# Performance work log

Hardware: AMD Instinct MI355X
Metric: run time of the kernel (lower is better)

## Reference

```python
import jax, jax.numpy as jnp
import numpy as np

N = 100000
E = 1600000
D_IN = 256
HID = 128
EPS = 1e-5


def setup_inputs() -> dict:
    key = jax.random.key(0)
    ks = jax.random.split(key, 8)
    x = jax.random.normal(ks[0], (N, D_IN), dtype=jnp.float32)
    edge_index = jax.random.randint(ks[1], (2, E), 0, N, dtype=jnp.int64)
    edge_weight = jax.random.uniform(ks[2], (E,), dtype=jnp.float32)
    # GCNConv lin weights (glorot-ish scale) + bias
    W1 = jax.random.normal(ks[3], (D_IN, HID), dtype=jnp.float32) / np.sqrt(D_IN)
    b1 = jnp.zeros((HID,), dtype=jnp.float32)
    W2 = jax.random.normal(ks[4], (HID, HID), dtype=jnp.float32) / np.sqrt(HID)
    b2 = jnp.zeros((HID,), dtype=jnp.float32)
    # BatchNorm affine params
    g1 = jnp.ones((HID,), dtype=jnp.float32)
    be1 = jnp.zeros((HID,), dtype=jnp.float32)
    g2 = jnp.ones((HID,), dtype=jnp.float32)
    be2 = jnp.zeros((HID,), dtype=jnp.float32)
    return {"x": x, "edge_index": edge_index, "edge_weight": edge_weight,
            "W1": W1, "b1": b1, "g1": g1, "be1": be1,
            "W2": W2, "b2": b2, "g2": g2, "be2": be2}


def _gcn_layer(h, src, dst, w, W, b):
    # GCNConv(add_self_loops=False, normalize=False):
    # h' = h @ W; out[i] = sum_{(j->i)} w_ji * h'[j]; out += b
    h = h @ W                                   # [N, out_dim]
    msg = w[:, None] * jnp.take(h, src, axis=0)  # [E, out_dim]
    agg = jax.ops.segment_sum(msg, dst, num_segments=N)
    return agg + b


def _bn(h, gamma, beta):
    # BatchNorm1d with batch statistics (biased variance), training-mode math
    mean = jnp.mean(h, axis=0)
    var = jnp.mean(jnp.square(h - mean), axis=0)
    return (h - mean) * jax.lax.rsqrt(var + EPS) * gamma + beta


def reference(x, edge_index, edge_weight, W1, b1, g1, be1, W2, b2, g2, be2):
    src = edge_index[0]
    dst = edge_index[1]
    h = _gcn_layer(x, src, dst, edge_weight, W1, b1)
    h = jax.nn.relu(_bn(h, g1, be1))
    h = _gcn_layer(h, src, dst, edge_weight, W2, b2)
    h = jax.nn.relu(_bn(h, g2, be2))  # last_activation=True
    return h
```

## Files before the change

### kernel.cpp

```cpp
#include <hip/hip_runtime.h>
#include <hip/hip_bf16.h>

#define NNODES 100000
#define DIN    256
#define NHID   128
#define EPS    1e-5f
#define SHIFT  9
#define NB2    ((NNODES + 511) >> SHIFT)
#define BCAP2  9216
#define CURPAD 16
#define PH     2048

typedef __attribute__((ext_vector_type(8))) short short8v;
typedef __attribute__((ext_vector_type(4))) float f32x4;

static __device__ __forceinline__ unsigned short f2bf(float v) {
    __hip_bfloat16 b = __float2bfloat16(v);
    return *reinterpret_cast<unsigned short*>(&b);
}
static __device__ __forceinline__ float bfhi2f(unsigned int u) {
    union { unsigned int i; float f; } x; x.i = u & 0xFFFF0000u; return x.f;
}
static __device__ __forceinline__ float bflo2f(unsigned int u) {
    union { unsigned int i; float f; } x; x.i = u << 16; return x.f;
}

__global__ __launch_bounds__(256) void prep_kernel(const float* __restrict__ W1,
                                                   const float* __restrict__ W2,
                                                   unsigned short* __restrict__ Wt1,
                                                   unsigned short* __restrict__ Wt2,
                                                   int* __restrict__ gcur,
                                                   float* __restrict__ sums) {
    int i = blockIdx.x * 256 + threadIdx.x;
    if (i < DIN * NHID) {
        const int k = i >> 7, c = i & 127;
        Wt1[c * DIN + k] = f2bf(W1[i]);
        return;
    }
    i -= DIN * NHID;
    if (i < NHID * NHID) {
        const int k = i >> 7, c = i & 127;
        Wt2[c * NHID + k] = f2bf(W2[i]);
        return;
    }
    i -= NHID * NHID;
    if (i < NB2 * CURPAD) { gcur[i] = 0; return; }
    i -= NB2 * CURPAD;
    if (i < 512) sums[i] = 0.f;
}

__global__ __launch_bounds__(256) void gemm1_part_kernel(
    const float* __restrict__ Af, const unsigned short* __restrict__ Wtb,
    unsigned short* __restrict__ C, int M, int ngemm,
    const int* __restrict__ src, const int* __restrict__ dst,
    const float* __restrict__ w, int* __restrict__ gcur,
    int2* __restrict__ bstage, int E) {
    struct GemmS { unsigned short As[2][64 * 40]; };
    struct PartS {
        int2 staged[PH];
        int hist[NB2], scn[NB2], cur[NB2], gbase[NB2];
        int pscan[256];
        unsigned char aux[PH];
    };
    __shared__ union { GemmS g; PartS p; } sm;

    const int t = threadIdx.x;
    if (blockIdx.x < ngemm) {
        constexpr int K = DIN;
        constexpr int NS = K / 32;
        constexpr int PADB = 40;
        const int wid = t >> 6;
        const int lane = t & 63;
        const int wr = wid >> 1, wc = wid & 1;
        const int l15 = lane & 15, g = lane >> 4;
        const int R0 = blockIdx.x * 64;
        const int RW = R0 + wr * 32;
        const int srow = t >> 2;
        const int scol = (t & 3) * 8;

        f32x4 acc[2][4] = {};

        auto STAGE = [&](int s, int buf) {
            const int k0 = s * 32;
            int grow = R0 + srow;
            grow = grow < M ? grow : M - 1;
            const float* p = Af + (size_t)grow * K + k0 + scol;
            const float4 v0 = *reinterpret_cast<const float4*>(p);
            const float4 v1 = *reinterpret_cast<const float4*>(p + 4);
            unsigned short bv[8];
            bv[0] = f2bf(v0.x); bv[1] = f2bf(v0.y); bv[2] = f2bf(v0.z); bv[3] = f2bf(v0.w);
            bv[4] = f2bf(v1.x); bv[5] = f2bf(v1.y); bv[6] = f2bf(v1.z); bv[7] = f2bf(v1.w);
            *reinterpret_cast<uint4*>(&sm.g.As[buf][srow * PADB + scol]) =
                *reinterpret_cast<const uint4*>(bv);
        };

        STAGE(0, 0);
        __syncthreads();

        for (int s = 0; s < NS; ++s) {
            if (s + 1 < NS) STAGE(s + 1, (s + 1) & 1);
            const unsigned short* ab = sm.g.As[s & 1];
            short8v b[4];
#pragma unroll
            for (int n = 0; n < 4; ++n) {
                const int col = wc * 64 + n * 16 + l15;
                b[n] = *reinterpret_cast<const short8v*>(&Wtb[(size_t)col * K + s * 32 + g * 8]);
            }
            short8v a[2];
#pragma unroll
            for (int m = 0; m < 2; ++m) {
                const int row = wr * 32 + m * 16 + l15;
                a[m] = *reinterpret_cast<const short8v*>(&ab[row * PADB + g * 8]);
            }
#pragma unroll
            for (int m = 0; m < 2; ++m)
#pragma unroll
                for (int n = 0; n < 4; ++n)
                    acc[m][n] = __builtin_amdgcn_mfma_f32_16x16x32_bf16(a[m], b[n], acc[m][n], 0, 0, 0);
            __syncthreads();
        }

#pragma unroll
        for (int m = 0; m < 2; ++m) {
#pragma unroll
            for (int q = 0; q < 4; ++q) {
                const int row = RW + m * 16 + g * 4 + q;
                if (row < M) {
                    unsigned short* cp = C + (size_t)row * NHID + wc * 64 + l15;
#pragma unroll
                    for (int n = 0; n < 4; ++n)
                        cp[n * 16] = f2bf(acc[m][n][q]);
                }
            }
        }
    } else {
        const int c = blockIdx.x - ngemm;
        const int e0 = c * PH;
        if (e0 >= E) return;
        const int cnt = min(PH, E - e0);
        for (int i = t; i < NB2; i += 256) sm.p.hist[i] = 0;
        __syncthreads();

        int2 pay[8];
        int bk[8];
#pragma unroll
        for (int j = 0; j < 8; ++j) {
            const int i = j * 256 + t;
            bk[j] = -1;
            if (i < cnt) {
                const int e = e0 + i;
                const int d = dst[e];
                bk[j] = d >> SHIFT;
                pay[j].x = src[e] | ((d & 511) << 17);
                pay[j].y = __float_as_int(w[e]);
                atomicAdd(&sm.p.hist[bk[j]], 1);
            }
        }
        __syncthreads();

        sm.p.pscan[t] = (t < NB2) ? sm.p.hist[t] : 0;
        __syncthreads();
        for (int off = 1; off < 256; off <<= 1) {
            const int v = (t >= off) ? sm.p.pscan[t - off] : 0;
            __syncthreads();
            sm.p.pscan[t] += v;
            __syncthreads();
        }
        if (t < NB2) {
            const int ex = sm.p.pscan[t] - sm.p.hist[t];
            sm.p.scn[t] = ex;
            sm.p.cur[t] = ex;
        }
        __syncthreads();

#pragma unroll
        for (int j = 0; j < 8; ++j) {
            if (bk[j] >= 0) {
                const int p = atomicAdd(&sm.p.cur[bk[j]], 1);
                sm.p.staged[p] = pay[j];
                sm.p.aux[p] = (unsigned char)bk[j];
            }
        }
        if (t < NB2 && sm.p.hist[t] > 0)
            sm.p.gbase[t] = atomicAdd(&gcur[t * CURPAD], sm.p.hist[t]);
        __syncthreads();

        for (int i = t; i < cnt; i += 256) {
            const int b = sm.p.aux[i];
            const int p = sm.p.gbase[b] + (i - sm.p.scn[b]);
            if (p < BCAP2) bstage[(size_t)b * BCAP2 + p] = sm.p.staged[i];
        }
    }
}

__global__ __launch_bounds__(512) void csr_kernel(const int* __restrict__ gcur,
                                                  const int2* __restrict__ bstage,
                                                  int2* __restrict__ row_be,
                                                  int2* __restrict__ s_iw) {
    const int b = blockIdx.x;
    const int t = threadIdx.x;
    int cnt = gcur[b * CURPAD];
    if (cnt > BCAP2) cnt = BCAP2;
    const int sbase = b * BCAP2;

    __shared__ int hist[512], cur[512];
    __shared__ int part[512];
    hist[t] = 0;
    __syncthreads();
    for (int i = t; i < cnt; i += 512)
        atomicAdd(&hist[(bstage[sbase + i].x >> 17) & 511], 1);
    __syncthreads();

    part[t] = hist[t];
    __syncthreads();
    for (int off = 1; off < 512; off <<= 1) {
        const int v = (t >= off) ? part[t - off] : 0;
        __syncthreads();
        part[t] += v;
        __syncthreads();
    }
    const int excl = part[t] - hist[t];
    cur[t] = excl;
    const int d = (b << SHIFT) + t;
    if (d < NNODES) {
        int2 be;
        be.x = sbase + excl;
        be.y = sbase + part[t];
        row_be[d] = be;
    }
    __syncthreads();

    for (int i = t; i < cnt; i += 512) {
        const int2 e = bstage[sbase + i];
        const int l = (e.x >> 17) & 511;
        const int p = atomicAdd(&cur[l], 1);
        int2 o;
        o.x = e.x & 0x1FFFF;
        o.y = e.y;
        s_iw[sbase + p] = o;
    }
}

#define EDGE_FMA(eN, vN)                                                        \
    {                                                                           \
        const float wN = __int_as_float(eN.y);                                  \
        acc[0] = fmaf(wN, bflo2f(vN.x), acc[0]);                                \
        acc[1] = fmaf(wN, bfhi2f(vN.x), acc[1]);                                \
        acc[2] = fmaf(wN, bflo2f(vN.y), acc[2]);                                \
        acc[3] = fmaf(wN, bfhi2f(vN.y), acc[3]);                                \
        acc[4] = fmaf(wN, bflo2f(vN.z), acc[4]);                                \
        acc[5] = fmaf(wN, bfhi2f(vN.z), acc[5]);                                \
        acc[6] = fmaf(wN, bflo2f(vN.w), acc[6]);                                \
        acc[7] = fmaf(wN, bfhi2f(vN.w), acc[7]);                                \
    }

__global__ __launch_bounds__(256) void aggregate_kernel(const unsigned short* __restrict__ hb,
                                                        const int2* __restrict__ row_be,
                                                        const int2* __restrict__ s_iw,
                                                        unsigned short* __restrict__ outB, int n) {
    const int wid = (blockIdx.x * 256 + threadIdx.x) >> 6;
    if (wid >= n) return;
    const int lane = threadIdx.x & 63;
    const int grp = lane >> 4;
    const int l16 = lane & 15;
    const int2 be = row_be[wid];
    const int end = be.y;

    float acc[8] = {};
    int j = be.x + grp;
    for (; j + 12 < end; j += 16) {
        const int2 e0 = s_iw[j];
        const int2 e1 = s_iw[j + 4];
        const int2 e2 = s_iw[j + 8];
        const int2 e3 = s_iw[j + 12];
        const uint4 v0 = *reinterpret_cast<const uint4*>(hb + (size_t)e0.x * NHID + l16 * 8);
        const uint4 v1 = *reinterpret_cast<const uint4*>(hb + (size_t)e1.x * NHID + l16 * 8);
        const uint4 v2 = *reinterpret_cast<const uint4*>(hb + (size_t)e2.x * NHID + l16 * 8);
        const uint4 v3 = *reinterpret_cast<const uint4*>(hb + (size_t)e3.x * NHID + l16 * 8);
        EDGE_FMA(e0, v0);
        EDGE_FMA(e1, v1);
        EDGE_FMA(e2, v2);
        EDGE_FMA(e3, v3);
    }
    for (; j < end; j += 4) {
        const int2 e0 = s_iw[j];
        const uint4 v0 = *reinterpret_cast<const uint4*>(hb + (size_t)e0.x * NHID + l16 * 8);
        EDGE_FMA(e0, v0);
    }
#pragma unroll
    for (int k = 0; k < 8; ++k) {
        acc[k] += __shfl_xor(acc[k], 16, 64);
        acc[k] += __shfl_xor(acc[k], 32, 64);
    }
    if (grp == 0) {
        unsigned short bv[8];
#pragma unroll
        for (int k = 0; k < 8; ++k) bv[k] = f2bf(acc[k]);
        *reinterpret_cast<uint4*>(outB + (size_t)wid * NHID + l16 * 8) =
            *reinterpret_cast<const uint4*>(bv);
    }
}

__global__ __launch_bounds__(256) void stats_kernel(const unsigned short* __restrict__ h,
                                                    float* __restrict__ sums, int nrows) {
    const int t = threadIdx.x;
    const int cp = t & 63;
    const int rg = t >> 6;
    float s0 = 0.f, s1 = 0.f, q0 = 0.f, q1 = 0.f;
    for (int r = blockIdx.x * 4 + rg; r < nrows; r += gridDim.x * 4) {
        const unsigned int v = *reinterpret_cast<const unsigned int*>(h + (size_t)r * NHID + cp * 2);
        const float a = bflo2f(v), b = bfhi2f(v);
        s0 += a; q0 = fmaf(a, a, q0);
        s1 += b; q1 = fmaf(b, b, q1);
    }
    __shared__ float ls[4][128], lq[4][128];
    ls[rg][cp * 2] = s0; ls[rg][cp * 2 + 1] = s1;
    lq[rg][cp * 2] = q0; lq[rg][cp * 2 + 1] = q1;
    __syncthreads();
    if (t < 128) {
        atomicAdd(&sums[t], ls[0][t] + ls[1][t] + ls[2][t] + ls[3][t]);
    } else {
        const int c = t - 128;
        atomicAdd(&sums[128 + c], lq[0][c] + lq[1][c] + lq[2][c] + lq[3][c]);
    }
}

__global__ __launch_bounds__(256) void mfma_gemm2(const unsigned short* __restrict__ Ab,
                                                  const unsigned short* __restrict__ Wtb,
                                                  const float* __restrict__ sums,
                                                  const float* __restrict__ gamma,
                                                  const float* __restrict__ beta,
                                                  unsigned short* __restrict__ C, int M) {
    constexpr int K = NHID;
    constexpr int NS = K / 32;
    constexpr int PADB = 40;
    __shared__ unsigned short As[2][64 * PADB];
    __shared__ float ssl[256];

    const int t = threadIdx.x;
    if (t < 128) {
        const float invN = 1.0f / (float)NNODES;
        const float mean = sums[t] * invN;
        const float var = sums[128 + t] * invN - mean * mean;
        const float scale = gamma[t] * rsqrtf(var + EPS);
        ssl[t] = scale;
        ssl[128 + t] = beta[t] - mean * scale;
    }
    __syncthreads();

    const int wid = t >> 6;
    const int lane = t & 63;
    const int wr = wid >> 1, wc = wid & 1;
    const int l15 = lane & 15, g = lane >> 4;
    const int R0 = blockIdx.x * 64;
    const int RW = R0 + wr * 32;
    const int srow = t >> 2;
    const int scol = (t & 3) * 8;

    f32x4 acc[2][4] = {};

    auto STAGE = [&](int s, int buf) {
        const int k0 = s * 32;
        int grow = R0 + srow;
        grow = grow < M ? grow : M - 1;
        const uint4 v = *reinterpret_cast<const uint4*>(Ab + (size_t)grow * K + k0 + scol);
        const float f[8] = {bflo2f(v.x), bfhi2f(v.x), bflo2f(v.y), bfhi2f(v.y),
                            bflo2f(v.z), bfhi2f(v.z), bflo2f(v.w), bfhi2f(v.w)};
        const int c0 = k0 + scol;
        unsigned short bv[8];
#pragma unroll
        for (int j = 0; j < 8; ++j)
            bv[j] = f2bf(fmaxf(fmaf(f[j], ssl[c0 + j], ssl[128 + c0 + j]), 0.f));
        *reinterpret_cast<uint4*>(&As[buf][srow * PADB + scol]) =
            *reinterpret_cast<const uint4*>(bv);
    };

    STAGE(0, 0);
    __syncthreads();

    for (int s = 0; s < NS; ++s) {
        if (s + 1 < NS) STAGE(s + 1, (s + 1) & 1);
        const unsigned short* ab = As[s & 1];
        short8v b[4];
#pragma unroll
        for (int n = 0; n < 4; ++n) {
            const int col = wc * 64 + n * 16 + l15;
            b[n] = *reinterpret_cast<const short8v*>(&Wtb[(size_t)col * K + s * 32 + g * 8]);
        }
        short8v a[2];
#pragma unroll
        for (int m = 0; m < 2; ++m) {
            const int row = wr * 32 + m * 16 + l15;
            a[m] = *reinterpret_cast<const short8v*>(&ab[row * PADB + g * 8]);
        }
#pragma unroll
        for (int m = 0; m < 2; ++m)
#pragma unroll
            for (int n = 0; n < 4; ++n)
                acc[m][n] = __builtin_amdgcn_mfma_f32_16x16x32_bf16(a[m], b[n], acc[m][n], 0, 0, 0);
        __syncthreads();
    }

#pragma unroll
    for (int m = 0; m < 2; ++m) {
#pragma unroll
        for (int q = 0; q < 4; ++q) {
            const int row = RW + m * 16 + g * 4 + q;
            if (row < M) {
                unsigned short* cp = C + (size_t)row * NHID + wc * 64 + l15;
#pragma unroll
                for (int n = 0; n < 4; ++n)
                    cp[n * 16] = f2bf(acc[m][n][q]);
            }
        }
    }
}

__global__ __launch_bounds__(256) void apply_kernel(const unsigned short* __restrict__ aggB,
                                                    const float* __restrict__ sums,
                                                    const float* __restrict__ gamma,
                                                    const float* __restrict__ beta,
                                                    float* __restrict__ out, int n8) {
    __shared__ float ss[256];
    const int t = threadIdx.x;
    if (t < 128) {
        const float invN = 1.0f / (float)NNODES;
        const float mean = sums[t] * invN;
        const float var = sums[128 + t] * invN - mean * mean;
        const float scale = gamma[t] * rsqrtf(var + EPS);
        ss[t] = scale;
        ss[128 + t] = beta[t] - mean * scale;
    }
    __syncthreads();
    const int idx = blockIdx.x * 256 + t;
    if (idx >= n8) return;
    const int c0 = (idx & 15) * 8;
    const uint4 v = reinterpret_cast<const uint4*>(aggB)[idx];
    const float f[8] = {bflo2f(v.x), bfhi2f(v.x), bflo2f(v.y), bfhi2f(v.y),
                        bflo2f(v.z), bfhi2f(v.z), bflo2f(v.w), bfhi2f(v.w)};
    float4 r0, r1;
    r0.x = fmaxf(fmaf(f[0], ss[c0],     ss[128 + c0]),     0.f);
    r0.y = fmaxf(fmaf(f[1], ss[c0 + 1], ss[128 + c0 + 1]), 0.f);
    r0.z = fmaxf(fmaf(f[2], ss[c0 + 2], ss[128 + c0 + 2]), 0.f);
    r0.w = fmaxf(fmaf(f[3], ss[c0 + 3], ss[128 + c0 + 3]), 0.f);
    r1.x = fmaxf(fmaf(f[4], ss[c0 + 4], ss[128 + c0 + 4]), 0.f);
    r1.y = fmaxf(fmaf(f[5], ss[c0 + 5], ss[128 + c0 + 5]), 0.f);
    r1.z = fmaxf(fmaf(f[6], ss[c0 + 6], ss[128 + c0 + 6]), 0.f);
    r1.w = fmaxf(fmaf(f[7], ss[c0 + 7], ss[128 + c0 + 7]), 0.f);
    reinterpret_cast<float4*>(out)[idx * 2] = r0;
    reinterpret_cast<float4*>(out)[idx * 2 + 1] = r1;
}

extern "C" void kernel_launch(void* const* d_in, const int* in_sizes, int n_in,
                              void* d_out, int out_size, void* d_ws, size_t ws_size,
                              hipStream_t stream) {
    const float* x   = (const float*)d_in[0];
    const int*   ei  = (const int*)d_in[1];
    const float* ew  = (const float*)d_in[2];
    const float* W1  = (const float*)d_in[3];
    const float* g1  = (const float*)d_in[5];
    const float* be1 = (const float*)d_in[6];
    const float* W2  = (const float*)d_in[7];
    const float* g2  = (const float*)d_in[9];
    const float* be2 = (const float*)d_in[10];
    float* out = (float*)d_out;

    const int M = NNODES;
    const int E = in_sizes[2];
    const int* src = ei;
    const int* dst = ei + E;

    unsigned short* hb   = (unsigned short*)d_ws;
    unsigned short* aggB = hb + (size_t)M * NHID;
    int2* bstage = (int2*)(aggB + (size_t)M * NHID);
    int2* s_iw   = bstage + (size_t)NB2 * BCAP2;
    int2* row_be = s_iw + (size_t)NB2 * BCAP2;
    int* gcur    = (int*)(row_be + NNODES);
    unsigned short* Wt1b = (unsigned short*)(gcur + NB2 * CURPAD);
    unsigned short* Wt2b = Wt1b + DIN * NHID;
    float* sums  = (float*)(Wt2b + NHID * NHID);

    const int gemm_grid = (M + 63) / 64;
    const int n8 = M * NHID / 8;
    const int app_grid = (n8 + 255) / 256;
    const int agg_grid = (M * 64 + 255) / 256;
    const int part_grid = (E + PH - 1) / PH;
    const int prep_tot = DIN * NHID + NHID * NHID + NB2 * CURPAD + 512;

    prep_kernel<<<(prep_tot + 255) / 256, 256, 0, stream>>>(W1, W2, Wt1b, Wt2b, gcur, sums);
    gemm1_part_kernel<<<gemm_grid + part_grid, 256, 0, stream>>>(
        x, Wt1b, hb, M, gemm_grid, src, dst, ew, gcur, bstage, E);
    csr_kernel<<<NB2, 512, 0, stream>>>(gcur, bstage, row_be, s_iw);

    aggregate_kernel<<<agg_grid, 256, 0, stream>>>(hb, row_be, s_iw, aggB, M);
    stats_kernel<<<1024, 256, 0, stream>>>(aggB, sums, M);

    mfma_gemm2<<<gemm_grid, 256, 0, stream>>>(aggB, Wt2b, sums, g1, be1, hb, M);
    aggregate_kernel<<<agg_grid, 256, 0, stream>>>(hb, row_be, s_iw, aggB, M);
    stats_kernel<<<1024, 256, 0, stream>>>(aggB, sums + 256, M);
    apply_kernel<<<app_grid, 256, 0, stream>>>(aggB, sums + 256, g2, be2, out, n8);
}
```

Before: 296.5 us.

## Stage full A tile into LDS upfront in both GEMMs, removing per-step barriers

Both GEMM kernels now issue every global load for the block's 64-row A tile at once into registers, convert to bf16, and write the whole K-wide tile into LDS before a single barrier. The previous double-buffered per-32-column staging, with a __syncthreads each step, is removed. This exposes more memory-level parallelism and cuts synchronization. The cost is more registers (up to 16 float4 per thread in gemm1) and larger LDS, which may lower occupancy and shares the union with the partition path.

Result: no change. 298.2 us (+0.6%).

```diff
diff --git a/kernel.cpp b/kernel.cpp
--- a/kernel.cpp
+++ b/kernel.cpp
@@ -55,7 +55,9 @@
     const int* __restrict__ src, const int* __restrict__ dst,
     const float* __restrict__ w, int* __restrict__ gcur,
     int2* __restrict__ bstage, int E) {
-    struct GemmS { unsigned short As[2][64 * 40]; };
+    constexpr int K1 = DIN;
+    constexpr int PADB1 = K1 + 8;
+    struct GemmS { unsigned short As[64 * PADB1]; };
     struct PartS {
         int2 staged[PH];
         int hist[NB2], scn[NB2], cur[NB2], gbase[NB2];
@@ -66,9 +68,7 @@
 
     const int t = threadIdx.x;
     if (blockIdx.x < ngemm) {
-        constexpr int K = DIN;
-        constexpr int NS = K / 32;
-        constexpr int PADB = 40;
+        constexpr int NS = K1 / 32;
         const int wid = t >> 6;
         const int lane = t & 63;
         const int wr = wid >> 1, wc = wid & 1;
@@ -78,46 +78,47 @@
         const int srow = t >> 2;
         const int scol = (t & 3) * 8;
 
+        int grow = R0 + srow;
+        grow = grow < M ? grow : M - 1;
+        const float* base = Af + (size_t)grow * K1 + scol;
+        float4 vr[2 * NS];
+#pragma unroll
+        for (int s = 0; s < NS; ++s) {
+            vr[2 * s]     = *reinterpret_cast<const float4*>(base + s * 32);
+            vr[2 * s + 1] = *reinterpret_cast<const float4*>(base + s * 32 + 4);
+        }
+#pragma unroll
+        for (int s = 0; s < NS; ++s) {
+            unsigned short bv[8];
+            bv[0] = f2bf(vr[2 * s].x);     bv[1] = f2bf(vr[2 * s].y);
+            bv[2] = f2bf(vr[2 * s].z);     bv[3] = f2bf(vr[2 * s].w);
+            bv[4] = f2bf(vr[2 * s + 1].x); bv[5] = f2bf(vr[2 * s + 1].y);
+            bv[6] = f2bf(vr[2 * s + 1].z); bv[7] = f2bf(vr[2 * s + 1].w);
+            *reinterpret_cast<uint4*>(&sm.g.As[srow * PADB1 + s * 32 + scol]) =
+                *reinterpret_cast<const uint4*>(bv);
+        }
+        __syncthreads();
+
         f32x4 acc[2][4] = {};
-
-        auto STAGE = [&](int s, int buf) {
-            const int k0 = s * 32;
-            int grow = R0 + srow;
-            grow = grow < M ? grow : M - 1;
-            const float* p = Af + (size_t)grow * K + k0 + scol;
-            const float4 v0 = *reinterpret_cast<const float4*>(p);
-            const float4 v1 = *reinterpret_cast<const float4*>(p + 4);
-            unsigned short bv[8];
-            bv[0] = f2bf(v0.x); bv[1] = f2bf(v0.y); bv[2] = f2bf(v0.z); bv[3] = f2bf(v0.w);
-            bv[4] = f2bf(v1.x); bv[5] = f2bf(v1.y); bv[6] = f2bf(v1.z); bv[7] = f2bf(v1.w);
-            *reinterpret_cast<uint4*>(&sm.g.As[buf][srow * PADB + scol]) =
-                *reinterpret_cast<const uint4*>(bv);
-        };
-
-        STAGE(0, 0);
-        __syncthreads();
-
+#pragma unroll
         for (int s = 0; s < NS; ++s) {
-            if (s + 1 < NS) STAGE(s + 1, (s + 1) & 1);
-            const unsigned short* ab = sm.g.As[s & 1];
             short8v b[4];
 #pragma unroll
             for (int n = 0; n < 4; ++n) {
                 const int col = wc * 64 + n * 16 + l15;
-                b[n] = *reinterpret_cast<const short8v*>(&Wtb[(size_t)col * K + s * 32 + g * 8]);
+                b[n] = *reinterpret_cast<const short8v*>(&Wtb[(size_t)col * K1 + s * 32 + g * 8]);
             }
             short8v a[2];
 #pragma unroll
             for (int m = 0; m < 2; ++m) {
                 const int row = wr * 32 + m * 16 + l15;
-                a[m] = *reinterpret_cast<const short8v*>(&ab[row * PADB + g * 8]);
+                a[m] = *reinterpret_cast<const short8v*>(&sm.g.As[row * PADB1 + s * 32 + g * 8]);
             }
 #pragma unroll
             for (int m = 0; m < 2; ++m)
 #pragma unroll
                 for (int n = 0; n < 4; ++n)
                     acc[m][n] = __builtin_amdgcn_mfma_f32_16x16x32_bf16(a[m], b[n], acc[m][n], 0, 0, 0);
-            __syncthreads();
         }
 
 #pragma unroll
@@ -333,8 +334,8 @@
                                                   unsigned short* __restrict__ C, int M) {
     constexpr int K = NHID;
     constexpr int NS = K / 32;
-    constexpr int PADB = 40;
-    __shared__ unsigned short As[2][64 * PADB];
+    constexpr int PADB = K + 8;
+    __shared__ unsigned short As[64 * PADB];
     __shared__ float ssl[256];
 
     const int t = threadIdx.x;
@@ -357,30 +358,30 @@
     const int srow = t >> 2;
     const int scol = (t & 3) * 8;
 
-    f32x4 acc[2][4] = {};
-
-    auto STAGE = [&](int s, int buf) {
-        const int k0 = s * 32;
-        int grow = R0 + srow;
-        grow = grow < M ? grow : M - 1;
-        const uint4 v = *reinterpret_cast<const uint4*>(Ab + (size_t)grow * K + k0 + scol);
-        const float f[8] = {bflo2f(v.x), bfhi2f(v.x), bflo2f(v.y), bfhi2f(v.y),
-                            bflo2f(v.z), bfhi2f(v.z), bflo2f(v.w), bfhi2f(v.w)};
-        const int c0 = k0 + scol;
+    int grow = R0 + srow;
+    grow = grow < M ? grow : M - 1;
+    const unsigned short* base = Ab + (size_t)grow * K + scol;
+    uint4 vr[NS];
+#pragma unroll
+    for (int s = 0; s < NS; ++s)
+        vr[s] = *reinterpret_cast<const uint4*>(base + s * 32);
+#pragma unroll
+    for (int s = 0; s < NS; ++s) {
+        const float f[8] = {bflo2f(vr[s].x), bfhi2f(vr[s].x), bflo2f(vr[s].y), bfhi2f(vr[s].y),
+                            bflo2f(vr[s].z), bfhi2f(vr[s].z), bflo2f(vr[s].w), bfhi2f(vr[s].w)};
+        const int c0 = s * 32 + scol;
         unsigned short bv[8];
 #pragma unroll
         for (int j = 0; j < 8; ++j)
             bv[j] = f2bf(fmaxf(fmaf(f[j], ssl[c0 + j], ssl[128 + c0 + j]), 0.f));
-        *reinterpret_cast<uint4*>(&As[buf][srow * PADB + scol]) =
+        *reinterpret_cast<uint4*>(&As[srow * PADB + s * 32 + scol]) =
             *reinterpret_cast<const uint4*>(bv);
-    };
-
-    STAGE(0, 0);
-    __syncthreads();
-
+    }
+    __syncthreads();
+
+    f32x4 acc[2][4] = {};
+#pragma unroll
     for (int s = 0; s < NS; ++s) {
-        if (s + 1 < NS) STAGE(s + 1, (s + 1) & 1);
-        const unsigned short* ab = As[s & 1];
         short8v b[4];
 #pragma unroll
         for (int n = 0; n < 4; ++n) {
@@ -391,14 +392,13 @@
 #pragma unroll
         for (int m = 0; m < 2; ++m) {
             const int row = wr * 32 + m * 16 + l15;
-            a[m] = *reinterpret_cast<const short8v*>(&ab[row * PADB + g * 8]);
+            a[m] = *reinterpret_cast<const short8v*>(&As[row * PADB + s * 32 + g * 8]);
         }
 #pragma unroll
         for (int m = 0; m < 2; ++m)
 #pragma unroll
             for (int n = 0; n < 4; ++n)
                 acc[m][n] = __builtin_amdgcn_mfma_f32_16x16x32_bf16(a[m], b[n], acc[m][n], 0, 0, 0);
-        __syncthreads();
     }
 
 #pragma unroll
```
